# Kernel tuning notes

Hardware: AMD Instinct MI355X
Metric: run time of the kernel (lower is better)

Reference implementation:

```python
import jax, jax.numpy as jnp
import numpy as np

B, C, N = 16, 3, 4096
K = 20
IN_CH, HID, OUT_CH = 2 * C, 64, 64
EPS = 1e-5
NEG_SLOPE = 0.2


def setup_inputs() -> dict:
    key = jax.random.key(0)
    ks = jax.random.split(key, 4)
    return {
        "x": jax.random.normal(ks[0], (B, C, N), dtype=jnp.float32),
        "W1": jax.random.normal(ks[1], (HID, IN_CH), dtype=jnp.float32) * 0.1,
        "W2": jax.random.normal(ks[2], (HID, HID), dtype=jnp.float32) * 0.1,
        "W3": jax.random.normal(ks[3], (OUT_CH, HID), dtype=jnp.float32) * 0.1,
        "g1": jnp.ones((HID,), jnp.float32),
        "b1": jnp.zeros((HID,), jnp.float32),
        "g2": jnp.ones((OUT_CH,), jnp.float32),
        "b2": jnp.zeros((OUT_CH,), jnp.float32),
    }


def _lrelu(y):
    return jnp.where(y > 0, y, NEG_SLOPE * y)


def _bn(y, gamma, beta):
    # training-mode BatchNorm2d: stats over all axes except channel (last here)
    mu = jnp.mean(y, axis=(0, 1, 2), keepdims=True)
    var = jnp.mean((y - mu) ** 2, axis=(0, 1, 2), keepdims=True)
    return (y - mu) * jax.lax.rsqrt(var + EPS) * gamma + beta


def _graph_feature(x, k):
    # x: [B, C, N] -> DGCNN edge features [B, N, k, 2C]
    xt = jnp.transpose(x, (0, 2, 1))  # [B, N, C]
    sq = jnp.sum(xt * xt, axis=-1)    # [B, N]
    # negative squared pairwise distance (top_k picks nearest, incl. self)
    neg_dist = 2.0 * jnp.einsum('bnc,bmc->bnm', xt, xt) - sq[:, :, None] - sq[:, None, :]
    _, idx = jax.lax.top_k(neg_dist, k)                 # [B, N, k]
    nbr = jax.vmap(lambda xb, ib: xb[ib])(xt, idx)      # [B, N, k, C] gather
    xc = jnp.broadcast_to(xt[:, :, None, :], nbr.shape)
    return jnp.concatenate([nbr - xc, xc], axis=-1)     # [B, N, k, 2C]


def reference(x, W1, W2, W3, g1, b1, g2, b2):
    f = _graph_feature(x, K)                    # [B, N, k, 2C]
    # 1x1 convs over channel axis (last), matching NCHW permute(0,3,2,1)
    y = jnp.einsum('bnkc,oc->bnko', f, W1)
    y = _bn(_lrelu(y), g1, b1)
    y = jnp.einsum('bnkc,oc->bnko', y, W2)
    y = _bn(_lrelu(y), g1, b1)                  # norm1 is reused (shared params)
    y = jnp.einsum('bnkc,oc->bnko', y, W3)
    y = _bn(_lrelu(y), g2, b2)
    y = jnp.max(y, axis=2)                      # max over k neighbors -> [B, N, out]
    return jnp.transpose(y, (0, 2, 1))          # [B, out, N]
```

## Files before the change

kernel.cpp:

```cpp
#include <hip/hip_runtime.h>
#include <math.h>

#define KNN 20
#define CNT_INV (1.0f / 1310720.0f)

typedef short bf16x8 __attribute__((ext_vector_type(8)));
typedef float f32x4  __attribute__((ext_vector_type(4)));

__device__ __forceinline__ short f2bf(float f) {
  unsigned u = __builtin_bit_cast(unsigned, f);
  u += 0x7FFFu + ((u >> 16) & 1u);
  return (short)(u >> 16);
}
__device__ __forceinline__ float lrelu(float y) { return y > 0.f ? y : 0.2f * y; }

__global__ __launch_bounds__(256) void xt4_kernel(const float* __restrict__ x,
                                                  float4* __restrict__ xt4) {
  const int t = blockIdx.x * 256 + threadIdx.x;
  const int b = t >> 12, m = t & 4095;
  const float* xb = x + (size_t)b * 12288;
  const float a = xb[m], c = xb[4096 + m], e = xb[8192 + m];
  xt4[t] = make_float4(a, c, e, a * a + c * c + e * e);
}

__global__ __launch_bounds__(256) void knn_kernel(const float4* __restrict__ xt4,
                                                  int* __restrict__ idx_out,
                                                  const float* __restrict__ W1,
                                                  float* __restrict__ s1buf) {
  __shared__ __align__(16) int hist[1024];
  __shared__ int sB[8];
  __shared__ int wcnt[4][4];
  __shared__ int slist[4][64];
  __shared__ int scnt[4];
  __shared__ int eidx[4][KNN];
  const int tid = threadIdx.x, lane = tid & 63, wid = tid >> 6;
  const int p0 = blockIdx.x * 4;
  const int b = p0 >> 12, n0 = p0 & 4095;
  const float4* xb4 = xt4 + (size_t)b * 4096;
  const float4 cp0 = xb4[n0], cp1 = xb4[n0 + 1], cp2 = xb4[n0 + 2], cp3 = xb4[n0 + 3];

  float w1r[6];
#pragma unroll
  for (int c = 0; c < 6; ++c) w1r[c] = W1[lane * 6 + c];

  float d0[16], d1[16], d2[16], d3[16];
#pragma unroll
  for (int i = 0; i < 16; ++i) {
    const float4 qv = xb4[i * 256 + tid];
    const float t0 = fmaf(cp0.x, qv.x, fmaf(cp0.y, qv.y, cp0.z * qv.z));
    const float t1 = fmaf(cp1.x, qv.x, fmaf(cp1.y, qv.y, cp1.z * qv.z));
    const float t2 = fmaf(cp2.x, qv.x, fmaf(cp2.y, qv.y, cp2.z * qv.z));
    const float t3 = fmaf(cp3.x, qv.x, fmaf(cp3.y, qv.y, cp3.z * qv.z));
    d0[i] = fmaf(-2.0f, t0, qv.w) + cp0.w;
    d1[i] = fmaf(-2.0f, t1, qv.w) + cp1.w;
    d2[i] = fmaf(-2.0f, t2, qv.w) + cp2.w;
    d3[i] = fmaf(-2.0f, t3, qv.w) + cp3.w;
  }

  *(int4*)&hist[tid * 4] = int4{0, 0, 0, 0};
  __syncthreads();
#pragma unroll
  for (int i = 0; i < 16; ++i) {
    if (d0[i] < 2.0f) atomicAdd(&hist[      (int)(d0[i] * 128.0f)], 1);
    if (d1[i] < 2.0f) atomicAdd(&hist[256 + (int)(d1[i] * 128.0f)], 1);
    if (d2[i] < 2.0f) atomicAdd(&hist[512 + (int)(d2[i] * 128.0f)], 1);
    if (d3[i] < 2.0f) atomicAdd(&hist[768 + (int)(d3[i] * 128.0f)], 1);
  }
  __syncthreads();
  {
    const int* h = &hist[wid * 256];
    int Bv = 256, cntv = 0, seam = 0;
#pragma unroll
    for (int c = 0; c < 4; ++c) {
      if (Bv == 256) {
        int s = h[c * 64 + lane];
#pragma unroll
        for (int off = 1; off < 64; off <<= 1) { const int t = __shfl_up(s, off); if (lane >= off) s += t; }
        s += seam;
        const unsigned long long m = __ballot(s >= 20);
        if (m) { const int l = __ffsll((long long)m) - 1; Bv = c * 64 + l; cntv = __shfl(s, l); }
        else seam = __shfl(s, 63);
      }
    }
    if (lane == 0) { sB[wid * 2] = Bv; sB[wid * 2 + 1] = cntv; }
  }
  __syncthreads();

  float lo0 = 0.f, R0 = 2.f, lo1 = 0.f, R1 = 2.f, lo2 = 0.f, R2 = 2.f, lo3 = 0.f, R3 = 2.f;
  int bef0 = 0, bef1 = 0, bef2 = 0, bef3 = 0;
  float Dedge0 = 1e30f, Dedge1 = 1e30f, Dedge2 = 1e30f, Dedge3 = 1e30f;
  bool dn0 = false, dn1 = false, dn2 = false, dn3 = false;
  {
    const float bw = 2.0f * (1.0f / 256.0f);
    bool zm0 = false, zm1 = false, zm2 = false, zm3 = false;
    {
      const int Bq = sB[0], cq = sB[1];
      if (Bq == 256) R0 = 32.0f;
      else {
        Dedge0 = (float)(Bq + 1) * bw;
        if (cq <= 48) dn0 = true;
        else { lo0 = (float)Bq * bw; R0 = bw; zm0 = true; }
      }
    }
    {
      const int Bq = sB[2], cq = sB[3];
      if (Bq == 256) R1 = 32.0f;
      else {
        Dedge1 = (float)(Bq + 1) * bw;
        if (cq <= 48) dn1 = true;
        else { lo1 = (float)Bq * bw; R1 = bw; zm1 = true; }
      }
    }
    {
      const int Bq = sB[4], cq = sB[5];
      if (Bq == 256) R2 = 32.0f;
      else {
        Dedge2 = (float)(Bq + 1) * bw;
        if (cq <= 48) dn2 = true;
        else { lo2 = (float)Bq * bw; R2 = bw; zm2 = true; }
      }
    }
    {
      const int Bq = sB[6], cq = sB[7];
      if (Bq == 256) R3 = 32.0f;
      else {
        Dedge3 = (float)(Bq + 1) * bw;
        if (cq <= 48) dn3 = true;
        else { lo3 = (float)Bq * bw; R3 = bw; zm3 = true; }
      }
    }
    if (zm0) {
      int c = 0;
#pragma unroll
      for (int i = 0; i < 16; ++i) c += (int)__popcll(__ballot(d0[i] < lo0));
      if (lane == 0) wcnt[0][wid] = c;
    }
    if (zm1) {
      int c = 0;
#pragma unroll
      for (int i = 0; i < 16; ++i) c += (int)__popcll(__ballot(d1[i] < lo1));
      if (lane == 0) wcnt[1][wid] = c;
    }
    if (zm2) {
      int c = 0;
#pragma unroll
      for (int i = 0; i < 16; ++i) c += (int)__popcll(__ballot(d2[i] < lo2));
      if (lane == 0) wcnt[2][wid] = c;
    }
    if (zm3) {
      int c = 0;
#pragma unroll
      for (int i = 0; i < 16; ++i) c += (int)__popcll(__ballot(d3[i] < lo3));
      if (lane == 0) wcnt[3][wid] = c;
    }
    if (zm0 | zm1 | zm2 | zm3) {
      __syncthreads();
      if (zm0) bef0 = wcnt[0][0] + wcnt[0][1] + wcnt[0][2] + wcnt[0][3];
      if (zm1) bef1 = wcnt[1][0] + wcnt[1][1] + wcnt[1][2] + wcnt[1][3];
      if (zm2) bef2 = wcnt[2][0] + wcnt[2][1] + wcnt[2][2] + wcnt[2][3];
      if (zm3) bef3 = wcnt[3][0] + wcnt[3][1] + wcnt[3][2] + wcnt[3][3];
    }
  }

  for (int pass = 1; pass < 6 && !(dn0 && dn1 && dn2 && dn3); ++pass) {
    *(int4*)&hist[tid * 4] = int4{0, 0, 0, 0};
    __syncthreads();
    const float sc0 = 256.0f / R0, sc1 = 256.0f / R1;
    const float sc2 = 256.0f / R2, sc3 = 256.0f / R3;
    if (!dn0) {
#pragma unroll
      for (int i = 0; i < 16; ++i) {
        const float rel = d0[i] - lo0;
        if (rel >= 0.0f && rel < R0) {
          int bin = (int)(rel * sc0); bin = bin > 255 ? 255 : bin;
          atomicAdd(&hist[bin], 1);
        }
      }
    }
    if (!dn1) {
#pragma unroll
      for (int i = 0; i < 16; ++i) {
        const float rel = d1[i] - lo1;
        if (rel >= 0.0f && rel < R1) {
          int bin = (int)(rel * sc1); bin = bin > 255 ? 255 : bin;
          atomicAdd(&hist[256 + bin], 1);
        }
      }
    }
    if (!dn2) {
#pragma unroll
      for (int i = 0; i < 16; ++i) {
        const float rel = d2[i] - lo2;
        if (rel >= 0.0f && rel < R2) {
          int bin = (int)(rel * sc2); bin = bin > 255 ? 255 : bin;
          atomicAdd(&hist[512 + bin], 1);
        }
      }
    }
    if (!dn3) {
#pragma unroll
      for (int i = 0; i < 16; ++i) {
        const float rel = d3[i] - lo3;
        if (rel >= 0.0f && rel < R3) {
          int bin = (int)(rel * sc3); bin = bin > 255 ? 255 : bin;
          atomicAdd(&hist[768 + bin], 1);
        }
      }
    }
    __syncthreads();
    {
      const bool skip = wid == 0 ? dn0 : wid == 1 ? dn1 : wid == 2 ? dn2 : dn3;
      if (!skip) {
        const int* h = &hist[wid * 256];
        int s0 = h[lane], s1 = h[64 + lane], s2 = h[128 + lane], s3 = h[192 + lane];
#pragma unroll
        for (int off = 1; off < 64; off <<= 1) { const int t = __shfl_up(s0, off); if (lane >= off) s0 += t; }
#pragma unroll
        for (int off = 1; off < 64; off <<= 1) { const int t = __shfl_up(s1, off); if (lane >= off) s1 += t; }
#pragma unroll
        for (int off = 1; off < 64; off <<= 1) { const int t = __shfl_up(s2, off); if (lane >= off) s2 += t; }
#pragma unroll
        for (int off = 1; off < 64; off <<= 1) { const int t = __shfl_up(s3, off); if (lane >= off) s3 += t; }
        s1 += __shfl(s0, 63);
        s2 += __shfl(s1, 63);
        s3 += __shfl(s2, 63);
        const int bef = wid == 0 ? bef0 : wid == 1 ? bef1 : wid == 2 ? bef2 : bef3;
        s0 += bef; s1 += bef; s2 += bef; s3 += bef;
        int B = 256, cnt = 0;
        unsigned long long m = __ballot(s0 >= 20);
        if (m) { const int l = __ffsll((long long)m) - 1; B = l; cnt = __shfl(s0, l); }
        else if ((m = __ballot(s1 >= 20)) != 0ull) { const int l = __ffsll((long long)m) - 1; B = 64 + l; cnt = __shfl(s1, l); }
        else if ((m = __ballot(s2 >= 20)) != 0ull) { const int l = __ffsll((long long)m) - 1; B = 128 + l; cnt = __shfl(s2, l); }
        else if ((m = __ballot(s3 >= 20)) != 0ull) { const int l = __ffsll((long long)m) - 1; B = 192 + l; cnt = __shfl(s3, l); }
        if (lane == 0) { sB[wid * 2] = B; sB[wid * 2 + 1] = cnt; }
      }
    }
    __syncthreads();
    bool zm0 = false, zm1 = false, zm2 = false, zm3 = false;
    if (!dn0) {
      const int Bq = sB[0], cq = sB[1];
      if (Bq == 256) R0 *= 16.0f;
      else {
        const float bw = R0 * (1.0f / 256.0f);
        Dedge0 = lo0 + (float)(Bq + 1) * bw;
        if (cq <= 48) dn0 = true;
        else { lo0 += (float)Bq * bw; R0 = bw; zm0 = true; }
      }
    }
    if (!dn1) {
      const int Bq = sB[2], cq = sB[3];
      if (Bq == 256) R1 *= 16.0f;
      else {
        const float bw = R1 * (1.0f / 256.0f);
        Dedge1 = lo1 + (float)(Bq + 1) * bw;
        if (cq <= 48) dn1 = true;
        else { lo1 += (float)Bq * bw; R1 = bw; zm1 = true; }
      }
    }
    if (!dn2) {
      const int Bq = sB[4], cq = sB[5];
      if (Bq == 256) R2 *= 16.0f;
      else {
        const float bw = R2 * (1.0f / 256.0f);
        Dedge2 = lo2 + (float)(Bq + 1) * bw;
        if (cq <= 48) dn2 = true;
        else { lo2 += (float)Bq * bw; R2 = bw; zm2 = true; }
      }
    }
    if (!dn3) {
      const int Bq = sB[6], cq = sB[7];
      if (Bq == 256) R3 *= 16.0f;
      else {
        const float bw = R3 * (1.0f / 256.0f);
        Dedge3 = lo3 + (float)(Bq + 1) * bw;
        if (cq <= 48) dn3 = true;
        else { lo3 += (float)Bq * bw; R3 = bw; zm3 = true; }
      }
    }
    if (zm0) {
      int c = 0;
#pragma unroll
      for (int i = 0; i < 16; ++i) c += (int)__popcll(__ballot(d0[i] < lo0));
      if (lane == 0) wcnt[0][wid] = c;
    }
    if (zm1) {
      int c = 0;
#pragma unroll
      for (int i = 0; i < 16; ++i) c += (int)__popcll(__ballot(d1[i] < lo1));
      if (lane == 0) wcnt[1][wid] = c;
    }
    if (zm2) {
      int c = 0;
#pragma unroll
      for (int i = 0; i < 16; ++i) c += (int)__popcll(__ballot(d2[i] < lo2));
      if (lane == 0) wcnt[2][wid] = c;
    }
    if (zm3) {
      int c = 0;
#pragma unroll
      for (int i = 0; i < 16; ++i) c += (int)__popcll(__ballot(d3[i] < lo3));
      if (lane == 0) wcnt[3][wid] = c;
    }
    if (zm0 | zm1 | zm2 | zm3) {
      __syncthreads();
      if (zm0) bef0 = wcnt[0][0] + wcnt[0][1] + wcnt[0][2] + wcnt[0][3];
      if (zm1) bef1 = wcnt[1][0] + wcnt[1][1] + wcnt[1][2] + wcnt[1][3];
      if (zm2) bef2 = wcnt[2][0] + wcnt[2][1] + wcnt[2][2] + wcnt[2][3];
      if (zm3) bef3 = wcnt[3][0] + wcnt[3][1] + wcnt[3][2] + wcnt[3][3];
    }
  }

  if (tid < 4) scnt[tid] = 0;
  __syncthreads();
  const float T0 = Dedge0 + 4e-3f, T1 = Dedge1 + 4e-3f;
  const float T2 = Dedge2 + 4e-3f, T3 = Dedge3 + 4e-3f;
#pragma unroll
  for (int i = 0; i < 16; ++i) {
    if (d0[i] < T0) {
      const int pos = atomicAdd(&scnt[0], 1);
      if (pos < 64) slist[0][pos] = i * 256 + tid;
    }
    if (d1[i] < T1) {
      const int pos = atomicAdd(&scnt[1], 1);
      if (pos < 64) slist[1][pos] = i * 256 + tid;
    }
    if (d2[i] < T2) {
      const int pos = atomicAdd(&scnt[2], 1);
      if (pos < 64) slist[2][pos] = i * 256 + tid;
    }
    if (d3[i] < T3) {
      const int pos = atomicAdd(&scnt[3], 1);
      if (pos < 64) slist[3][pos] = i * 256 + tid;
    }
  }
  __syncthreads();

  const float4 cp = wid == 0 ? cp0 : wid == 1 ? cp1 : wid == 2 ? cp2 : cp3;
  {
    const int s = min(scnt[wid], 64);
    int myi = -1; double myd = -1.0e300;
    if (lane < s) {
      myi = slist[wid][lane];
      const float4 av = xb4[myi];
      const double c0 = (double)cp.x, c1 = (double)cp.y, c2 = (double)cp.z;
      const double a0 = (double)av.x, a1 = (double)av.y, a2 = (double)av.z;
      const double dot = c0 * a0 + c1 * a1 + c2 * a2;
      const double sqm = a0 * a0 + a1 * a1 + a2 * a2;
      const double sn  = c0 * c0 + c1 * c1 + c2 * c2;
      myd = (2.0 * dot - sn) - sqm;
    }
    int rank = 0;
    for (int j = 0; j < s; ++j) {
      const double od = __shfl(myd, j);
      const int    oi = __shfl(myi, j);
      if (od > myd || (od == myd && oi < myi)) ++rank;
    }
    if (lane < s && rank < KNN) {
      idx_out[(p0 + wid) * KNN + rank] = myi;
      eidx[wid][rank] = myi;
    }
  }

  const float base1 = (w1r[3] - w1r[0]) * cp.x + (w1r[4] - w1r[1]) * cp.y +
                      (w1r[5] - w1r[2]) * cp.z;
  float sm = 0.f, sq = 0.f;
#pragma unroll
  for (int t = 0; t < KNN; ++t) {
    const int kk = eidx[wid][t];
    const float4 qv = xb4[kk];
    float y = fmaf(w1r[0], qv.x, fmaf(w1r[1], qv.y, fmaf(w1r[2], qv.z, base1)));
    y = lrelu(y);
    sm += y; sq = fmaf(y, y, sq);
  }
  float* bk = s1buf + (size_t)((p0 + wid) & 255) * 128;
  atomicAdd(&bk[lane], sm);
  atomicAdd(&bk[64 + lane], sq);
}

template <int STAGE, int MINW>
__global__ __launch_bounds__(256, MINW) void stage_kernel(
    const float4* __restrict__ xt4, const int* __restrict__ nbr,
    const float* __restrict__ W1,
    const float* __restrict__ w2ft, const float* __restrict__ b2f,
    const float* __restrict__ w3ft, const float* __restrict__ b3f,
    float* __restrict__ sumO, float* __restrict__ sqO,
    float* __restrict__ mx, float* __restrict__ mn) {
  __shared__ float pts[4][96];
  __shared__ float W1T[384];
  __shared__ short abuf[4][2048];
  __shared__ float redS[256], redQ[256];

  const int tid = threadIdx.x, wave = tid >> 6, lane = tid & 63;
  const int q = lane >> 4, cc = lane & 15;

  for (int i = tid; i < 384; i += 256) W1T[i] = W1[(i & 63) * 6 + (i >> 6)];
  __syncthreads();

  float w1r[6];
#pragma unroll
  for (int c = 0; c < 6; ++c) w1r[c] = W1T[c * 64 + lane];

  bf16x8 w2f[2][4];
#pragma unroll
  for (int kt = 0; kt < 2; ++kt)
#pragma unroll
    for (int nt = 0; nt < 4; ++nt)
#pragma unroll
      for (int j = 0; j < 8; ++j)
        w2f[kt][nt][j] = f2bf(w2ft[(kt * 32 + q * 8 + j) * 64 + nt * 16 + cc]);
  float bias2v[4];
#pragma unroll
  for (int nt = 0; nt < 4; ++nt) bias2v[nt] = b2f[nt * 16 + cc];

  bf16x8 w3f[2][4];
  float bias3v[4];
  if (STAGE == 3) {
#pragma unroll
    for (int kt = 0; kt < 2; ++kt)
#pragma unroll
      for (int nt = 0; nt < 4; ++nt)
#pragma unroll
        for (int j = 0; j < 8; ++j)
          w3f[kt][nt][j] = f2bf(w3ft[(kt * 32 + q * 8 + j) * 64 + nt * 16 + cc]);
#pragma unroll
    for (int nt = 0; nt < 4; ++nt) bias3v[nt] = b3f[nt * 16 + cc];
  }

  const int kt1 = lane >> 5, q1 = (lane & 31) >> 3, j1 = lane & 7;
  short* ab = abuf[wave];
  const bf16x8* ab8 = (const bf16x8*)ab;
  float* pw = pts[wave];

  float s_s[4] = {0.f, 0.f, 0.f, 0.f}, s_q[4] = {0.f, 0.f, 0.f, 0.f};
  const int wgid = blockIdx.x * 4 + wave;

  const int stepN = 8192 * KNN;
  const int* nbp = nbr + (size_t)wgid * KNN + lane;
  const float4* xb0 = xt4 + (size_t)(wgid >> 12) * 4096;
  const int nn = wgid & 4095;
  int kkB = 0;
  float4 g;
  if (lane < KNN) {
    const int kkA = nbp[0];
    g = xb0[kkA];
    kkB = nbp[stepN];
  } else if (lane == KNN) {
    g = xb0[nn];
  }
  const int* nbp2 = nbp + 2 * stepN;
  const float4* xbn = xb0 + 8192;

  for (int it = 0; it < 8; ++it) {
    const int p = wgid + it * 8192;
    if (lane <= KNN) *(float4*)&pw[lane * 4] = g;
    float4 gn = g; int kkC = kkB;
    if (it < 7 && lane <= KNN) gn = (lane < KNN) ? xbn[kkB] : xbn[nn];
    if (it < 6 && lane < KNN) kkC = nbp2[0];

    const float cx0 = pw[80], cx1 = pw[81], cx2 = pw[82];
    const float base1 = (w1r[3] - w1r[0]) * cx0 + (w1r[4] - w1r[1]) * cx1 +
                        (w1r[5] - w1r[2]) * cx2;

#pragma unroll
    for (int k = 0; k < KNN; ++k) {
      const float4 pk = *(const float4*)&pw[k * 4];
      float y = fmaf(w1r[0], pk.x, fmaf(w1r[1], pk.y, fmaf(w1r[2], pk.z, base1)));
      y = lrelu(y);
      ab[(((k >> 4) * 2 + kt1) * 64 + q1 * 16 + (k & 15)) * 8 + j1] = f2bf(y);
    }

    f32x4 acc2[2][4];
#pragma unroll
    for (int mt = 0; mt < 2; ++mt)
#pragma unroll
      for (int nt = 0; nt < 4; ++nt)
        acc2[mt][nt] = f32x4{bias2v[nt], bias2v[nt], bias2v[nt], bias2v[nt]};
#pragma unroll
    for (int kt = 0; kt < 2; ++kt) {
      const bf16x8 a0 = ab8[(0 * 2 + kt) * 64 + lane];
      const bf16x8 a1 = ab8[(1 * 2 + kt) * 64 + lane];
#pragma unroll
      for (int nt = 0; nt < 4; ++nt) {
        acc2[0][nt] = __builtin_amdgcn_mfma_f32_16x16x32_bf16(a0, w2f[kt][nt], acc2[0][nt], 0, 0, 0);
        acc2[1][nt] = __builtin_amdgcn_mfma_f32_16x16x32_bf16(a1, w2f[kt][nt], acc2[1][nt], 0, 0, 0);
      }
    }

    if (STAGE == 2) {
#pragma unroll
      for (int mt = 0; mt < 2; ++mt)
#pragma unroll
        for (int nt = 0; nt < 4; ++nt)
#pragma unroll
          for (int r = 0; r < 4; ++r) {
            if (mt == 1 && q != 0) continue;
            const float y = lrelu(acc2[mt][nt][r]);
            s_s[nt] += y; s_q[nt] += y * y;
          }
    } else {
#pragma unroll
      for (int mt = 0; mt < 2; ++mt)
#pragma unroll
        for (int nt = 0; nt < 4; ++nt) {
          const int kt3 = nt >> 1;
          const int q3 = (nt & 1) * 2 + (cc >> 3);
          const int j3 = cc & 7;
#pragma unroll
          for (int r = 0; r < 4; ++r) {
            if (mt == 1 && q != 0) continue;
            const float y = lrelu(acc2[mt][nt][r]);
            ab[((mt * 2 + kt3) * 64 + q3 * 16 + q * 4 + r) * 8 + j3] = f2bf(y);
          }
        }

      f32x4 acc3[2][4];
#pragma unroll
      for (int mt = 0; mt < 2; ++mt)
#pragma unroll
        for (int nt = 0; nt < 4; ++nt)
          acc3[mt][nt] = f32x4{bias3v[nt], bias3v[nt], bias3v[nt], bias3v[nt]};
#pragma unroll
      for (int kt = 0; kt < 2; ++kt) {
        const bf16x8 a0 = ab8[(0 * 2 + kt) * 64 + lane];
        const bf16x8 a1 = ab8[(1 * 2 + kt) * 64 + lane];
#pragma unroll
        for (int nt = 0; nt < 4; ++nt) {
          acc3[0][nt] = __builtin_amdgcn_mfma_f32_16x16x32_bf16(a0, w3f[kt][nt], acc3[0][nt], 0, 0, 0);
          acc3[1][nt] = __builtin_amdgcn_mfma_f32_16x16x32_bf16(a1, w3f[kt][nt], acc3[1][nt], 0, 0, 0);
        }
      }

      float vmx[4], vmn[4];
#pragma unroll
      for (int nt = 0; nt < 4; ++nt) { vmx[nt] = -INFINITY; vmn[nt] = INFINITY; }
#pragma unroll
      for (int mt = 0; mt < 2; ++mt)
#pragma unroll
        for (int nt = 0; nt < 4; ++nt)
#pragma unroll
          for (int r = 0; r < 4; ++r) {
            if (mt == 1 && q != 0) continue;
            const float y = lrelu(acc3[mt][nt][r]);
            s_s[nt] += y; s_q[nt] += y * y;
            vmx[nt] = fmaxf(vmx[nt], y); vmn[nt] = fminf(vmn[nt], y);
          }
#pragma unroll
      for (int nt = 0; nt < 4; ++nt) {
        vmx[nt] = fmaxf(vmx[nt], __shfl_xor(vmx[nt], 16));
        vmx[nt] = fmaxf(vmx[nt], __shfl_xor(vmx[nt], 32));
        vmn[nt] = fminf(vmn[nt], __shfl_xor(vmn[nt], 16));
        vmn[nt] = fminf(vmn[nt], __shfl_xor(vmn[nt], 32));
      }
      const float omx = q == 0 ? vmx[0] : q == 1 ? vmx[1] : q == 2 ? vmx[2] : vmx[3];
      const float omn = q == 0 ? vmn[0] : q == 1 ? vmn[1] : q == 2 ? vmn[2] : vmn[3];
      mx[(size_t)p * 64 + lane] = omx;
      mn[(size_t)p * 64 + lane] = omn;
    }

    g = gn; kkB = kkC; nbp2 += stepN; xbn += 8192;
  }

#pragma unroll
  for (int nt = 0; nt < 4; ++nt) {
    s_s[nt] += __shfl_xor(s_s[nt], 16); s_s[nt] += __shfl_xor(s_s[nt], 32);
    s_q[nt] += __shfl_xor(s_q[nt], 16); s_q[nt] += __shfl_xor(s_q[nt], 32);
  }
  const float ms = q == 0 ? s_s[0] : q == 1 ? s_s[1] : q == 2 ? s_s[2] : s_s[3];
  const float mq = q == 0 ? s_q[0] : q == 1 ? s_q[1] : q == 2 ? s_q[2] : s_q[3];
  redS[tid] = ms; redQ[tid] = mq;
  __syncthreads();
  if (tid < 64) {
    const float s  = redS[tid] + redS[64 + tid] + redS[128 + tid] + redS[192 + tid];
    const float qq = redQ[tid] + redQ[64 + tid] + redQ[128 + tid] + redQ[192 + tid];
    atomicAdd(&sumO[tid], s);
    atomicAdd(&sqO[tid], qq);
  }
}

__global__ void fold1_kernel(const float* __restrict__ s1buf,
                             const float* __restrict__ g, const float* __restrict__ bt,
                             const float* __restrict__ W,
                             float* __restrict__ WfT, float* __restrict__ bf) {
  __shared__ float s[64], t[64];
  const int o = threadIdx.x;
  float sm = 0.f, qq = 0.f;
  for (int k = 0; k < 256; ++k) { sm += s1buf[k * 128 + o]; qq += s1buf[k * 128 + 64 + o]; }
  const float mu = sm * CNT_INV;
  const float var = qq * CNT_INV - mu * mu;
  const float sc = g[o] / sqrtf(var + 1e-5f);
  s[o] = sc; t[o] = bt[o] - mu * sc;
  __syncthreads();
  float acc = 0.f;
  for (int c = 0; c < 64; ++c) {
    const float w = W[o * 64 + c];
    WfT[c * 64 + o] = w * s[c];
    acc += w * t[c];
  }
  bf[o] = acc;
}

__global__ void fold_kernel(const float* __restrict__ sum, const float* __restrict__ sq,
                            const float* __restrict__ g, const float* __restrict__ bt,
                            const float* __restrict__ W,
                            float* __restrict__ WfT, float* __restrict__ bf) {
  __shared__ float s[64], t[64];
  const int o = threadIdx.x;
  const float mu = sum[o] * CNT_INV;
  const float var = sq[o] * CNT_INV - mu * mu;
  const float sc = g[o] / sqrtf(var + 1e-5f);
  s[o] = sc; t[o] = bt[o] - mu * sc;
  __syncthreads();
  float acc = 0.f;
  for (int c = 0; c < 64; ++c) {
    const float w = W[o * 64 + c];
    WfT[c * 64 + o] = w * s[c];
    acc += w * t[c];
  }
  bf[o] = acc;
}

__global__ void fold3_kernel(const float* __restrict__ sum, const float* __restrict__ sq,
                             const float* __restrict__ g, const float* __restrict__ bt,
                             float* __restrict__ s3, float* __restrict__ t3) {
  const int o = threadIdx.x;
  const float mu = sum[o] * CNT_INV;
  const float var = sq[o] * CNT_INV - mu * mu;
  const float sc = g[o] / sqrtf(var + 1e-5f);
  s3[o] = sc; t3[o] = bt[o] - mu * sc;
}

__global__ __launch_bounds__(256) void final_kernel(
    const float* __restrict__ mx, const float* __restrict__ mn,
    const float* __restrict__ s3, const float* __restrict__ t3,
    float* __restrict__ out) {
  __shared__ float tmx[64][65], tmn[64][65];
  __shared__ float ss[64], tt[64];
  const int tid = threadIdx.x;
  const int P = blockIdx.x * 64;
  const int b = P >> 12, nb = P & 4095;
  if (tid < 64) { ss[tid] = s3[tid]; tt[tid] = t3[tid]; }
#pragma unroll
  for (int r = 0; r < 16; ++r) {
    const int idx = r * 256 + tid;
    const int pl = idx >> 6, ch = idx & 63;
    const size_t src = ((size_t)(P + pl)) * 64 + ch;
    tmx[pl][ch] = mx[src];
    tmn[pl][ch] = mn[src];
  }
  __syncthreads();
  const int nl = tid & 63;
#pragma unroll
  for (int r = 0; r < 16; ++r) {
    const int o = (tid >> 6) + r * 4;
    const float sc = ss[o];
    const float v = sc >= 0.f ? tmx[nl][o] : tmn[nl][o];
    out[(size_t)b * 262144 + (size_t)o * 4096 + nb + nl] = sc * v + tt[o];
  }
}

extern "C" void kernel_launch(void* const* d_in, const int* in_sizes, int n_in,
                              void* d_out, int out_size, void* d_ws, size_t ws_size,
                              hipStream_t stream) {
  const float* x  = (const float*)d_in[0];
  const float* W1 = (const float*)d_in[1];
  const float* W2 = (const float*)d_in[2];
  const float* W3 = (const float*)d_in[3];
  const float* g1 = (const float*)d_in[4];
  const float* b1 = (const float*)d_in[5];
  const float* g2 = (const float*)d_in[6];
  const float* b2 = (const float*)d_in[7];
  float* out = (float*)d_out;

  char* ws = (char*)d_ws;
  float4* xt4 = (float4*)ws;
  int* idx = (int*)(ws + 1048576);
  float* F = (float*)(ws + 6291456);
  float* sum2 = F + 0,   * sq2 = F + 64;
  float* sum3 = F + 128, * sq3 = F + 192;
  float* s1buf = F + 256;
  float* W2fT = F + 33024;
  float* b2f  = F + 37120;
  float* W3fT = F + 37184;
  float* b3f  = F + 41280;
  float* s3   = F + 41344;
  float* t3   = F + 41408;
  float* mx = (float*)(ws + 6457344);
  float* mn = mx + (size_t)16 * 4096 * 64;

  hipMemsetAsync(F, 0, 33024 * sizeof(float), stream);

  xt4_kernel<<<256, 256, 0, stream>>>(x, xt4);
  knn_kernel<<<16384, 256, 0, stream>>>(xt4, idx, W1, s1buf);
  fold1_kernel<<<1, 64, 0, stream>>>(s1buf, g1, b1, W2, W2fT, b2f);
  stage_kernel<2, 3><<<2048, 256, 0, stream>>>(xt4, idx, W1, W2fT, b2f, nullptr,
                                               nullptr, sum2, sq2, nullptr, nullptr);
  fold_kernel<<<1, 64, 0, stream>>>(sum2, sq2, g1, b1, W3, W3fT, b3f);
  stage_kernel<3, 2><<<2048, 256, 0, stream>>>(xt4, idx, W1, W2fT, b2f, W3fT,
                                               b3f, sum3, sq3, mx, mn);
  fold3_kernel<<<1, 64, 0, stream>>>(sum3, sq3, g2, b2, s3, t3);
  final_kernel<<<1024, 256, 0, stream>>>(mx, mn, s3, t3, out);
}
```

Before: 519.1 us.

## Materialize stage-2 activations in bf16 and run stage 3 from stored buffer

Stage 2 now writes its post-LeakyReLU activations (pre-BN, folded later) as bf16 fragments to a large workspace buffer. A new stage3y kernel reads them back and performs only the W3 MFMA, stats and max/min. This avoids recomputing the gather, layer 1 and layer 2 in stage 3. The cost is about 268 MB of extra global write and read traffic. It only applies when the workspace is large enough, otherwise the old recompute path runs.

```diff
diff --git a/kernel.cpp b/kernel.cpp
--- a/kernel.cpp
+++ b/kernel.cpp
@@ -377,14 +377,15 @@
   atomicAdd(&bk[64 + lane], sq);
 }
 
-template <int STAGE, int MINW>
+template <int STAGE, int MINW, bool Y2>
 __global__ __launch_bounds__(256, MINW) void stage_kernel(
     const float4* __restrict__ xt4, const int* __restrict__ nbr,
     const float* __restrict__ W1,
     const float* __restrict__ w2ft, const float* __restrict__ b2f,
     const float* __restrict__ w3ft, const float* __restrict__ b3f,
     float* __restrict__ sumO, float* __restrict__ sqO,
-    float* __restrict__ mx, float* __restrict__ mn) {
+    float* __restrict__ mx, float* __restrict__ mn,
+    bf16x8* __restrict__ y2out) {
   __shared__ float pts[4][96];
   __shared__ float W1T[384];
   __shared__ short abuf[4][2048];
@@ -497,6 +498,25 @@
             const float y = lrelu(acc2[mt][nt][r]);
             s_s[nt] += y; s_q[nt] += y * y;
           }
+      if constexpr (Y2) {
+#pragma unroll
+        for (int mt = 0; mt < 2; ++mt)
+#pragma unroll
+          for (int nt = 0; nt < 4; ++nt) {
+            const int kt3 = nt >> 1;
+            const int q3 = (nt & 1) * 2 + (cc >> 3);
+            const int j3 = cc & 7;
+#pragma unroll
+            for (int r = 0; r < 4; ++r) {
+              if (mt == 1 && q != 0) continue;
+              const float y = lrelu(acc2[mt][nt][r]);
+              ab[((mt * 2 + kt3) * 64 + q3 * 16 + q * 4 + r) * 8 + j3] = f2bf(y);
+            }
+          }
+        bf16x8* yp = y2out + (size_t)p * 256 + lane;
+#pragma unroll
+        for (int f = 0; f < 4; ++f) yp[f * 64] = ab8[f * 64 + lane];
+      }
     } else {
 #pragma unroll
       for (int mt = 0; mt < 2; ++mt)
@@ -558,6 +578,101 @@
     }
 
     g = gn; kkB = kkC; nbp2 += stepN; xbn += 8192;
+  }
+
+#pragma unroll
+  for (int nt = 0; nt < 4; ++nt) {
+    s_s[nt] += __shfl_xor(s_s[nt], 16); s_s[nt] += __shfl_xor(s_s[nt], 32);
+    s_q[nt] += __shfl_xor(s_q[nt], 16); s_q[nt] += __shfl_xor(s_q[nt], 32);
+  }
+  const float ms = q == 0 ? s_s[0] : q == 1 ? s_s[1] : q == 2 ? s_s[2] : s_s[3];
+  const float mq = q == 0 ? s_q[0] : q == 1 ? s_q[1] : q == 2 ? s_q[2] : s_q[3];
+  redS[tid] = ms; redQ[tid] = mq;
+  __syncthreads();
+  if (tid < 64) {
+    const float s  = redS[tid] + redS[64 + tid] + redS[128 + tid] + redS[192 + tid];
+    const float qq = redQ[tid] + redQ[64 + tid] + redQ[128 + tid] + redQ[192 + tid];
+    atomicAdd(&sumO[tid], s);
+    atomicAdd(&sqO[tid], qq);
+  }
+}
+
+__global__ __launch_bounds__(256, 3) void stage3y_kernel(
+    const bf16x8* __restrict__ y2, const float* __restrict__ w3ft,
+    const float* __restrict__ b3f, float* __restrict__ sumO,
+    float* __restrict__ sqO, float* __restrict__ mx, float* __restrict__ mn) {
+  __shared__ float redS[256], redQ[256];
+  const int tid = threadIdx.x, wave = tid >> 6, lane = tid & 63;
+  const int q = lane >> 4, cc = lane & 15;
+
+  bf16x8 w3f[2][4];
+#pragma unroll
+  for (int kt = 0; kt < 2; ++kt)
+#pragma unroll
+    for (int nt = 0; nt < 4; ++nt)
+#pragma unroll
+      for (int j = 0; j < 8; ++j)
+        w3f[kt][nt][j] = f2bf(w3ft[(kt * 32 + q * 8 + j) * 64 + nt * 16 + cc]);
+  float bias3v[4];
+#pragma unroll
+  for (int nt = 0; nt < 4; ++nt) bias3v[nt] = b3f[nt * 16 + cc];
+
+  float s_s[4] = {0.f, 0.f, 0.f, 0.f}, s_q[4] = {0.f, 0.f, 0.f, 0.f};
+  const int wgid = blockIdx.x * 4 + wave;
+
+  const bf16x8* yp = y2 + (size_t)wgid * 256 + lane;
+  bf16x8 f0 = yp[0], f1 = yp[64], f2 = yp[128], f3 = yp[192];
+
+  for (int it = 0; it < 8; ++it) {
+    const int p = wgid + it * 8192;
+    const bf16x8 c0 = f0, c1 = f1, c2 = f2, c3 = f3;
+    if (it < 7) {
+      const bf16x8* ypn = y2 + (size_t)(p + 8192) * 256 + lane;
+      f0 = ypn[0]; f1 = ypn[64]; f2 = ypn[128]; f3 = ypn[192];
+    }
+
+    f32x4 acc3[2][4];
+#pragma unroll
+    for (int mt = 0; mt < 2; ++mt)
+#pragma unroll
+      for (int nt = 0; nt < 4; ++nt)
+        acc3[mt][nt] = f32x4{bias3v[nt], bias3v[nt], bias3v[nt], bias3v[nt]};
+#pragma unroll
+    for (int nt = 0; nt < 4; ++nt) {
+      acc3[0][nt] = __builtin_amdgcn_mfma_f32_16x16x32_bf16(c0, w3f[0][nt], acc3[0][nt], 0, 0, 0);
+      acc3[1][nt] = __builtin_amdgcn_mfma_f32_16x16x32_bf16(c2, w3f[0][nt], acc3[1][nt], 0, 0, 0);
+    }
+#pragma unroll
+    for (int nt = 0; nt < 4; ++nt) {
+      acc3[0][nt] = __builtin_amdgcn_mfma_f32_16x16x32_bf16(c1, w3f[1][nt], acc3[0][nt], 0, 0, 0);
+      acc3[1][nt] = __builtin_amdgcn_mfma_f32_16x16x32_bf16(c3, w3f[1][nt], acc3[1][nt], 0, 0, 0);
+    }
+
+    float vmx[4], vmn[4];
+#pragma unroll
+    for (int nt = 0; nt < 4; ++nt) { vmx[nt] = -INFINITY; vmn[nt] = INFINITY; }
+#pragma unroll
+    for (int mt = 0; mt < 2; ++mt)
+#pragma unroll
+      for (int nt = 0; nt < 4; ++nt)
+#pragma unroll
+        for (int r = 0; r < 4; ++r) {
+          if (mt == 1 && q != 0) continue;
+          const float y = lrelu(acc3[mt][nt][r]);
+          s_s[nt] += y; s_q[nt] += y * y;
+          vmx[nt] = fmaxf(vmx[nt], y); vmn[nt] = fminf(vmn[nt], y);
+        }
+#pragma unroll
+    for (int nt = 0; nt < 4; ++nt) {
+      vmx[nt] = fmaxf(vmx[nt], __shfl_xor(vmx[nt], 16));
+      vmx[nt] = fmaxf(vmx[nt], __shfl_xor(vmx[nt], 32));
+      vmn[nt] = fminf(vmn[nt], __shfl_xor(vmn[nt], 16));
+      vmn[nt] = fminf(vmn[nt], __shfl_xor(vmn[nt], 32));
+    }
+    const float omx = q == 0 ? vmx[0] : q == 1 ? vmx[1] : q == 2 ? vmx[2] : vmx[3];
+    const float omn = q == 0 ? vmn[0] : q == 1 ? vmn[1] : q == 2 ? vmn[2] : vmn[3];
+    mx[(size_t)p * 64 + lane] = omx;
+    mn[(size_t)p * 64 + lane] = omn;
   }
 
 #pragma unroll
@@ -686,17 +801,28 @@
   float* t3   = F + 41408;
   float* mx = (float*)(ws + 6457344);
   float* mn = mx + (size_t)16 * 4096 * 64;
+  const size_t Y2_OFF  = 40013824;
+  const size_t Y2_SIZE = (size_t)65536 * 4096;
+  bf16x8* y2 = (bf16x8*)(ws + Y2_OFF);
+  const bool useY2 = ws_size >= Y2_OFF + Y2_SIZE;
 
   hipMemsetAsync(F, 0, 33024 * sizeof(float), stream);
 
   xt4_kernel<<<256, 256, 0, stream>>>(x, xt4);
   knn_kernel<<<16384, 256, 0, stream>>>(xt4, idx, W1, s1buf);
   fold1_kernel<<<1, 64, 0, stream>>>(s1buf, g1, b1, W2, W2fT, b2f);
-  stage_kernel<2, 3><<<2048, 256, 0, stream>>>(xt4, idx, W1, W2fT, b2f, nullptr,
-                                               nullptr, sum2, sq2, nullptr, nullptr);
-  fold_kernel<<<1, 64, 0, stream>>>(sum2, sq2, g1, b1, W3, W3fT, b3f);
-  stage_kernel<3, 2><<<2048, 256, 0, stream>>>(xt4, idx, W1, W2fT, b2f, W3fT,
-                                               b3f, sum3, sq3, mx, mn);
+  if (useY2) {
+    stage_kernel<2, 3, true><<<2048, 256, 0, stream>>>(
+        xt4, idx, W1, W2fT, b2f, nullptr, nullptr, sum2, sq2, nullptr, nullptr, y2);
+    fold_kernel<<<1, 64, 0, stream>>>(sum2, sq2, g1, b1, W3, W3fT, b3f);
+    stage3y_kernel<<<2048, 256, 0, stream>>>(y2, W3fT, b3f, sum3, sq3, mx, mn);
+  } else {
+    stage_kernel<2, 3, false><<<2048, 256, 0, stream>>>(
+        xt4, idx, W1, W2fT, b2f, nullptr, nullptr, sum2, sq2, nullptr, nullptr, nullptr);
+    fold_kernel<<<1, 64, 0, stream>>>(sum2, sq2, g1, b1, W3, W3fT, b3f);
+    stage_kernel<3, 2, false><<<2048, 256, 0, stream>>>(
+        xt4, idx, W1, W2fT, b2f, W3fT, b3f, sum3, sq3, mx, mn, nullptr);
+  }
   fold3_kernel<<<1, 64, 0, stream>>>(sum3, sq3, g2, b2, s3, t3);
   final_kernel<<<1024, 256, 0, stream>>>(mx, mn, s3, t3, out);
 }
```

New measurement: 522.2 us. About the same (+0.6%).
